# Kernel optimization log

Measured on AMD Instinct MI355X. Metric: run time of the kernel, lower is better.

Reference implementation:

```python
import jax, jax.numpy as jnp
import numpy as np

LN_EPS = 1e-5


def setup_inputs() -> dict:
    key = jax.random.key(0)
    ks = jax.random.split(key, 6)
    B, I, H = 16384, 512, 512
    x = jax.random.normal(ks[0], (B, I), dtype=jnp.float32)
    h_prev = jax.random.normal(ks[1], (B, H), dtype=jnp.float32)
    c_prev = jax.random.normal(ks[2], (B, H), dtype=jnp.float32)
    # packed gate weights in i|f|g|o order (equivalent to 8 separate matmuls)
    W_i = jax.random.normal(ks[3], (I, 4 * H), dtype=jnp.float32) * (1.0 / np.sqrt(I))
    W_h = jax.random.normal(ks[4], (H, 4 * H), dtype=jnp.float32) * (1.0 / np.sqrt(H))
    # biases: b_i=0, b_f=1, b_g=0, b_o=0 as in the torch module
    b = jnp.concatenate([jnp.zeros(H), jnp.ones(H), jnp.zeros(H), jnp.zeros(H)]).astype(jnp.float32)
    ln_weight = jnp.ones((H,), dtype=jnp.float32)
    ln_bias = jnp.zeros((H,), dtype=jnp.float32)
    return {"x": x, "h_prev": h_prev, "c_prev": c_prev, "W_i": W_i, "W_h": W_h,
            "b": b, "ln_weight": ln_weight, "ln_bias": ln_bias}


def layer_norm(h, w, bias):
    mu = jnp.mean(h, axis=-1, keepdims=True)
    var = jnp.var(h, axis=-1, keepdims=True)
    return (h - mu) * jax.lax.rsqrt(var + LN_EPS) * w + bias


def reference(x, h_prev, c_prev, W_i, W_h, b, ln_weight, ln_bias):
    H = h_prev.shape[-1]
    # two fused GEMMs covering all 4 gates: [B, 4H]
    gates = x @ W_i + h_prev @ W_h + b
    i, f, g, o = jnp.split(gates, 4, axis=-1)
    i = jax.nn.sigmoid(i)
    f = jax.nn.sigmoid(f)
    g = jnp.tanh(g)
    o = jax.nn.sigmoid(o)
    c = f * c_prev + i * g
    h = o * jnp.tanh(c)
    h = layer_norm(h, ln_weight, ln_bias)
    return (h, c)
```

## Files before the change

kernel.cpp:

```cpp
#include <hip/hip_runtime.h>
#include <cstdint>
#include <cstddef>

typedef unsigned short ushort_t;
typedef __attribute__((ext_vector_type(8))) short bf16x8;
typedef __attribute__((ext_vector_type(4))) float f32x4;

#define MROWS 16384
#define KDIM  1024
#define NDIM  2048
#define HDIM  512
#define NTILE 16

static __device__ __forceinline__ unsigned short f2bf(float f) {
    unsigned int u = __float_as_uint(f);
    u += 0x7fffu + ((u >> 16) & 1u);
    return (unsigned short)(u >> 16);
}

static __device__ __forceinline__ float sigmoid_f(float x) {
    return 1.0f / (1.0f + __expf(-x));
}
static __device__ __forceinline__ float tanh_f(float x) {
    float t = __expf(2.0f * x);
    return 1.0f - 2.0f / (t + 1.0f);
}

#define PACK_ABLK 2048
#define PACK_STRIDE (PACK_ABLK * 256)
__global__ __launch_bounds__(256) void pack_ab(const float* __restrict__ x,
                                               const float* __restrict__ hp,
                                               const float* __restrict__ Wi,
                                               const float* __restrict__ Wh,
                                               ushort_t* __restrict__ A,
                                               ushort_t* __restrict__ Bt) {
    __shared__ ushort_t sm[64][72];
    const int tid = threadIdx.x;
    if (blockIdx.x < PACK_ABLK) {
        int g = blockIdx.x * 256 + tid;
        float4 v[8];
#pragma unroll
        for (int s = 0; s < 4; ++s) {
            int c = g + s * PACK_STRIDE;
            int row = c >> 7;
            int kc = (c & 127) << 3;
            const float* src = (kc < 512) ? (x + (size_t)row * 512 + kc)
                                          : (hp + (size_t)row * 512 + (kc - 512));
            v[2 * s]     = ((const float4*)src)[0];
            v[2 * s + 1] = ((const float4*)src)[1];
        }
#pragma unroll
        for (int s = 0; s < 4; ++s) {
            int c = g + s * PACK_STRIDE;
            int row = c >> 7;
            int kc = (c & 127) << 3;
            ushort_t o[8] __attribute__((aligned(16)));
            o[0] = f2bf(v[2 * s].x);     o[1] = f2bf(v[2 * s].y);
            o[2] = f2bf(v[2 * s].z);     o[3] = f2bf(v[2 * s].w);
            o[4] = f2bf(v[2 * s + 1].x); o[5] = f2bf(v[2 * s + 1].y);
            o[6] = f2bf(v[2 * s + 1].z); o[7] = f2bf(v[2 * s + 1].w);
            *((uint4*)(A + (size_t)row * KDIM + kc)) = *((const uint4*)o);
        }
    } else {
        int b2 = blockIdx.x - PACK_ABLK;
        int kt = b2 >> 5;
        int ct = b2 & 31;
        const float* W = (kt < 8) ? (Wi + (size_t)(kt * 64) * NDIM)
                                  : (Wh + (size_t)((kt - 8) * 64) * NDIM);
        int c0 = (tid & 15) * 4;
        int r0 = tid >> 4;
#pragma unroll
        for (int r = 0; r < 4; ++r) {
            int krow = r * 16 + r0;
            float4 v = *((const float4*)(W + (size_t)krow * NDIM + ct * 64 + c0));
            sm[krow][c0 + 0] = f2bf(v.x);
            sm[krow][c0 + 1] = f2bf(v.y);
            sm[krow][c0 + 2] = f2bf(v.z);
            sm[krow][c0 + 3] = f2bf(v.w);
        }
        __syncthreads();
        int g = (ct * 64) >> 9;
        int h0 = ct * 64 - g * 512;
#pragma unroll
        for (int q = tid; q < 512; q += 256) {
            int cc = q >> 3;
            int kc = (q & 7) * 8;
            ushort_t o[8] __attribute__((aligned(16)));
#pragma unroll
            for (int j = 0; j < 8; ++j) o[j] = sm[kc + j][cc];
            int np = 4 * (h0 + cc) + g;
            *((uint4*)(Bt + (size_t)np * KDIM + kt * 64 + kc)) = *((const uint4*)o);
        }
    }
}

__global__ __launch_bounds__(512, 2) void gemm_cell(const ushort_t* __restrict__ A,
                                                    const ushort_t* __restrict__ Bt,
                                                    const float* __restrict__ b,
                                                    const float* __restrict__ c_prev,
                                                    float* __restrict__ h_out,
                                                    float* __restrict__ c_out) {
    __shared__ ushort_t lds[2][32768];

    const int tid  = threadIdx.x;
    const int w    = tid >> 6;
    const int lane = tid & 63;
    const int mi   = w >> 2;
    const int nj   = w & 3;
    int bid = blockIdx.x;
    int lid = (bid & 7) * 64 + (bid >> 3);
    const int m0 = (lid >> 3) * 256;
    const int n0 = (lid & 7) * 256;
    const int lr   = lane & 15;
    const int quad = lane >> 4;
    const int sw   = lr & 7;

    const int trow0 = tid >> 3;
    const int chg   = (tid & 7) ^ (trow0 & 7);
    const size_t a_base = (size_t)(m0 + trow0) * KDIM + chg * 8;
    const size_t b_base = (size_t)(n0 + trow0) * KDIM + chg * 8;
    const int    l_base = tid * 16;

#define STAGE_A_SLOT(kt, bufi, r_)                                              \
    __builtin_amdgcn_global_load_lds(                                           \
        (const __attribute__((address_space(1))) void*)(A + a_base +            \
            (size_t)(kt) * 64 + (size_t)(r_) * 64 * KDIM),                      \
        (__attribute__((address_space(3))) void*)((char*)&lds[bufi][0] +        \
            l_base + (r_) * 8192), 16, 0, 0)
#define STAGE_B_SLOT(kt, bufi, r_)                                              \
    __builtin_amdgcn_global_load_lds(                                           \
        (const __attribute__((address_space(1))) void*)(Bt + b_base +           \
            (size_t)(kt) * 64 + (size_t)(r_) * 64 * KDIM),                      \
        (__attribute__((address_space(3))) void*)((char*)&lds[bufi][16384] +    \
            l_base + (r_) * 8192), 16, 0, 0)

    f32x4 acc[8][4];
#pragma unroll
    for (int i = 0; i < 8; ++i)
#pragma unroll
        for (int j = 0; j < 4; ++j) acc[i][j] = (f32x4){0.f, 0.f, 0.f, 0.f};

    STAGE_A_SLOT(0, 0, 0); STAGE_A_SLOT(0, 0, 1); STAGE_A_SLOT(0, 0, 2); STAGE_A_SLOT(0, 0, 3);
    STAGE_B_SLOT(0, 0, 0); STAGE_B_SLOT(0, 0, 1); STAGE_B_SLOT(0, 0, 2); STAGE_B_SLOT(0, 0, 3);
    STAGE_A_SLOT(1, 1, 0); STAGE_A_SLOT(1, 1, 1); STAGE_A_SLOT(1, 1, 2); STAGE_A_SLOT(1, 1, 3);
    STAGE_B_SLOT(1, 1, 0); STAGE_B_SLOT(1, 1, 1); STAGE_B_SLOT(1, 1, 2); STAGE_B_SLOT(1, 1, 3);
    asm volatile("s_waitcnt vmcnt(8)\n\ts_barrier" ::: "memory");

#define TILE(t_, BUF_) do {                                                         \
    const ushort_t* Ab_ = &lds[BUF_][0];                                            \
    const ushort_t* Bb_ = &lds[BUF_][16384];                                        \
    bf16x8 af[4][2], b0v[2][2], b1v[2][2];                                          \
                    \
    _Pragma("unroll")                                                               \
    for (int t2 = 0; t2 < 4; ++t2) {                                                \
        int ra = mi * 128 + t2 * 16 + lr;                                           \
        af[t2][0] = *((const bf16x8*)(Ab_ + (ra * 8 + (quad ^ sw)) * 8));           \
        af[t2][1] = *((const bf16x8*)(Ab_ + (ra * 8 + ((4 + quad) ^ sw)) * 8));     \
    }                                                                               \
    _Pragma("unroll")                                                               \
    for (int j = 0; j < 2; ++j) {                                                   \
        int rb = nj * 64 + j * 16 + lr;                                             \
        b0v[j][0] = *((const bf16x8*)(Bb_ + (rb * 8 + (quad ^ sw)) * 8));           \
        b0v[j][1] = *((const bf16x8*)(Bb_ + (rb * 8 + ((4 + quad) ^ sw)) * 8));     \
    }                                                                               \
    __builtin_amdgcn_s_setprio(1);                                                  \
    _Pragma("unroll")                                                               \
    for (int t2 = 0; t2 < 4; ++t2)                                                  \
        _Pragma("unroll")                                                           \
        for (int j = 0; j < 2; ++j) {                                               \
            acc[t2][j] = __builtin_amdgcn_mfma_f32_16x16x32_bf16(                   \
                af[t2][0], b0v[j][0], acc[t2][j], 0, 0, 0);                         \
            acc[t2][j] = __builtin_amdgcn_mfma_f32_16x16x32_bf16(                   \
                af[t2][1], b0v[j][1], acc[t2][j], 0, 0, 0);                         \
        }                                                                           \
    __builtin_amdgcn_s_setprio(0);                                                  \
    asm volatile("s_barrier" ::: "memory");           \
    if ((t_) < NTILE - 2) { STAGE_A_SLOT((t_) + 2, BUF_, 0);                        \
                            STAGE_A_SLOT((t_) + 2, BUF_, 2); }                      \
                                            \
    _Pragma("unroll")                                                               \
    for (int j = 0; j < 2; ++j) {                                                   \
        int rb = nj * 64 + (j + 2) * 16 + lr;                                       \
        b1v[j][0] = *((const bf16x8*)(Bb_ + (rb * 8 + (quad ^ sw)) * 8));           \
        b1v[j][1] = *((const bf16x8*)(Bb_ + (rb * 8 + ((4 + quad) ^ sw)) * 8));     \
    }                                                                               \
    __builtin_amdgcn_s_setprio(1);                                                  \
    _Pragma("unroll")                                                               \
    for (int t2 = 0; t2 < 4; ++t2)                                                  \
        _Pragma("unroll")                                                           \
        for (int j = 0; j < 2; ++j) {                                               \
            acc[t2][j + 2] = __builtin_amdgcn_mfma_f32_16x16x32_bf16(               \
                af[t2][0], b1v[j][0], acc[t2][j + 2], 0, 0, 0);                     \
            acc[t2][j + 2] = __builtin_amdgcn_mfma_f32_16x16x32_bf16(               \
                af[t2][1], b1v[j][1], acc[t2][j + 2], 0, 0, 0);                     \
        }                                                                           \
    __builtin_amdgcn_s_setprio(0);                                                  \
    asm volatile("s_barrier" ::: "memory");            \
    if ((t_) < NTILE - 2) { STAGE_B_SLOT((t_) + 2, BUF_, 0);                        \
                            STAGE_B_SLOT((t_) + 2, BUF_, 1); }                      \
          \
    _Pragma("unroll")                                                               \
    for (int t2 = 0; t2 < 4; ++t2) {                                                \
        int ra = mi * 128 + (t2 + 4) * 16 + lr;                                     \
        af[t2][0] = *((const bf16x8*)(Ab_ + (ra * 8 + (quad ^ sw)) * 8));           \
        af[t2][1] = *((const bf16x8*)(Ab_ + (ra * 8 + ((4 + quad) ^ sw)) * 8));     \
    }                                                                               \
    __builtin_amdgcn_s_setprio(1);                                                  \
    _Pragma("unroll")                                                               \
    for (int t2 = 0; t2 < 4; ++t2)                                                  \
        _Pragma("unroll")                                                           \
        for (int j = 0; j < 2; ++j) {                                               \
            acc[t2 + 4][j] = __builtin_amdgcn_mfma_f32_16x16x32_bf16(               \
                af[t2][0], b0v[j][0], acc[t2 + 4][j], 0, 0, 0);                     \
            acc[t2 + 4][j] = __builtin_amdgcn_mfma_f32_16x16x32_bf16(               \
                af[t2][1], b0v[j][1], acc[t2 + 4][j], 0, 0, 0);                     \
        }                                                                           \
    __builtin_amdgcn_s_setprio(0);                                                  \
    asm volatile("s_waitcnt lgkmcnt(0)\n\ts_barrier" ::: "memory");         \
    if ((t_) < NTILE - 2) { STAGE_B_SLOT((t_) + 2, BUF_, 2);                        \
                            STAGE_B_SLOT((t_) + 2, BUF_, 3);                        \
                            STAGE_A_SLOT((t_) + 2, BUF_, 1);                        \
                            STAGE_A_SLOT((t_) + 2, BUF_, 3); }                      \
               \
    __builtin_amdgcn_s_setprio(1);                                                  \
    _Pragma("unroll")                                                               \
    for (int t2 = 0; t2 < 4; ++t2)                                                  \
        _Pragma("unroll")                                                           \
        for (int j = 0; j < 2; ++j) {                                               \
            acc[t2 + 4][j + 2] = __builtin_amdgcn_mfma_f32_16x16x32_bf16(           \
                af[t2][0], b1v[j][0], acc[t2 + 4][j + 2], 0, 0, 0);                 \
            acc[t2 + 4][j + 2] = __builtin_amdgcn_mfma_f32_16x16x32_bf16(           \
                af[t2][1], b1v[j][1], acc[t2 + 4][j + 2], 0, 0, 0);                 \
        }                                                                           \
    __builtin_amdgcn_s_setprio(0);                                                  \
    if ((t_) < NTILE - 2) {                                                         \
             \
        asm volatile("s_waitcnt vmcnt(8)\n\ts_barrier" ::: "memory");               \
    } else if ((t_) == NTILE - 2) {                                                 \
        asm volatile("s_waitcnt vmcnt(0)\n\ts_barrier" ::: "memory");               \
    } else {                                                                        \
        asm volatile("s_waitcnt lgkmcnt(0)\n\ts_barrier" ::: "memory");             \
    }                                                                               \
} while (0)

    for (int tp = 0; tp < NTILE / 2; ++tp) {
        TILE(2 * tp, 0);
        TILE(2 * tp + 1, 1);
    }
#undef TILE
#undef STAGE_A_SLOT
#undef STAGE_B_SLOT

    float* scr = (float*)&lds[0][0] + w * 1024;
    const int rr = lane >> 2;
    const int hg0 = ((n0 + nj * 64) >> 2) + (lane & 3) * 4;
    const float4 bi4 = *((const float4*)(b + hg0));
    const float4 bff = *((const float4*)(b + 512 + hg0));
    const float4 bgg = *((const float4*)(b + 1024 + hg0));
    const float4 boo = *((const float4*)(b + 1536 + hg0));
    const float bi[4] = {bi4.x, bi4.y, bi4.z, bi4.w};
    const float bfv[4] = {bff.x, bff.y, bff.z, bff.w};
    const float bg[4] = {bgg.x, bgg.y, bgg.z, bgg.w};
    const float bo[4] = {boo.x, boo.y, boo.z, boo.w};

#pragma unroll
    for (int tm = 0; tm < 8; ++tm) {
#pragma unroll
        for (int tn = 0; tn < 4; ++tn) {
            int c = tn * 16 + lr;
#pragma unroll
            for (int rg = 0; rg < 4; ++rg) {
                int r = quad * 4 + rg;
                int blk = (c >> 2) ^ r;
                scr[r * 64 + blk * 4 + (c & 3)] = acc[tm][tn][rg];
            }
        }
        float4 gv[4];
#pragma unroll
        for (int j = 0; j < 4; ++j) {
            int cb = (lane & 3) * 4 + j;
            gv[j] = *((const float4*)(scr + rr * 64 + (cb ^ rr) * 4));
        }
        int grow = m0 + mi * 128 + tm * 16 + rr;
        float4 cp4 = *((const float4*)(c_prev + (size_t)grow * HDIM + hg0));
        const float cpv[4] = {cp4.x, cp4.y, cp4.z, cp4.w};
        float cn[4], hv[4];
#pragma unroll
        for (int j = 0; j < 4; ++j) {
            float iv = sigmoid_f(gv[j].x + bi[j]);
            float fv = sigmoid_f(gv[j].y + bfv[j]);
            float g2 = tanh_f(gv[j].z + bg[j]);
            float ov = sigmoid_f(gv[j].w + bo[j]);
            cn[j] = fv * cpv[j] + iv * g2;
            hv[j] = ov * tanh_f(cn[j]);
        }
        float4 cno = {cn[0], cn[1], cn[2], cn[3]};
        float4 hvo = {hv[0], hv[1], hv[2], hv[3]};
        *((float4*)(c_out + (size_t)grow * HDIM + hg0)) = cno;
        *((float4*)(h_out + (size_t)grow * HDIM + hg0)) = hvo;
    }
}

__global__ __launch_bounds__(256) void ln_kernel(float* __restrict__ h,
                                                 const float* __restrict__ lw,
                                                 const float* __restrict__ lb) {
    int w = threadIdx.x >> 6;
    int lane = threadIdx.x & 63;
    int r0 = blockIdx.x * 4 + w;
    int r1 = r0 + (MROWS >> 1);
    float* p0 = h + (size_t)r0 * HDIM + lane * 8;
    float* p1 = h + (size_t)r1 * HDIM + lane * 8;
    float4 a0 = ((const float4*)p0)[0];
    float4 c0 = ((const float4*)p0)[1];
    float4 a1 = ((const float4*)p1)[0];
    float4 c1 = ((const float4*)p1)[1];
    const float* wp = lw + lane * 8;
    const float* bp = lb + lane * 8;
    float4 w0 = ((const float4*)wp)[0];
    float4 w1 = ((const float4*)wp)[1];
    float4 b0 = ((const float4*)bp)[0];
    float4 b1 = ((const float4*)bp)[1];

    float s0  = a0.x + a0.y + a0.z + a0.w + c0.x + c0.y + c0.z + c0.w;
    float ss0 = a0.x * a0.x + a0.y * a0.y + a0.z * a0.z + a0.w * a0.w +
                c0.x * c0.x + c0.y * c0.y + c0.z * c0.z + c0.w * c0.w;
    float s1  = a1.x + a1.y + a1.z + a1.w + c1.x + c1.y + c1.z + c1.w;
    float ss1 = a1.x * a1.x + a1.y * a1.y + a1.z * a1.z + a1.w * a1.w +
                c1.x * c1.x + c1.y * c1.y + c1.z * c1.z + c1.w * c1.w;
#pragma unroll
    for (int off = 32; off > 0; off >>= 1) {
        s0  += __shfl_xor(s0, off);
        ss0 += __shfl_xor(ss0, off);
        s1  += __shfl_xor(s1, off);
        ss1 += __shfl_xor(ss1, off);
    }
    float mu0 = s0 * (1.0f / 512.0f);
    float var0 = ss0 * (1.0f / 512.0f) - mu0 * mu0;
    float rstd0 = rsqrtf(var0 + 1e-5f);
    float mu1 = s1 * (1.0f / 512.0f);
    float var1 = ss1 * (1.0f / 512.0f) - mu1 * mu1;
    float rstd1 = rsqrtf(var1 + 1e-5f);

    a0.x = (a0.x - mu0) * rstd0 * w0.x + b0.x;
    a0.y = (a0.y - mu0) * rstd0 * w0.y + b0.y;
    a0.z = (a0.z - mu0) * rstd0 * w0.z + b0.z;
    a0.w = (a0.w - mu0) * rstd0 * w0.w + b0.w;
    c0.x = (c0.x - mu0) * rstd0 * w1.x + b1.x;
    c0.y = (c0.y - mu0) * rstd0 * w1.y + b1.y;
    c0.z = (c0.z - mu0) * rstd0 * w1.z + b1.z;
    c0.w = (c0.w - mu0) * rstd0 * w1.w + b1.w;
    a1.x = (a1.x - mu1) * rstd1 * w0.x + b0.x;
    a1.y = (a1.y - mu1) * rstd1 * w0.y + b0.y;
    a1.z = (a1.z - mu1) * rstd1 * w0.z + b0.z;
    a1.w = (a1.w - mu1) * rstd1 * w0.w + b0.w;
    c1.x = (c1.x - mu1) * rstd1 * w1.x + b1.x;
    c1.y = (c1.y - mu1) * rstd1 * w1.y + b1.y;
    c1.z = (c1.z - mu1) * rstd1 * w1.z + b1.z;
    c1.w = (c1.w - mu1) * rstd1 * w1.w + b1.w;
    ((float4*)p0)[0] = a0;
    ((float4*)p0)[1] = c0;
    ((float4*)p1)[0] = a1;
    ((float4*)p1)[1] = c1;
}

extern "C" void kernel_launch(void* const* d_in, const int* in_sizes, int n_in,
                              void* d_out, int out_size, void* d_ws, size_t ws_size,
                              hipStream_t stream) {
    const float* x      = (const float*)d_in[0];
    const float* h_prev = (const float*)d_in[1];
    const float* c_prev = (const float*)d_in[2];
    const float* W_i    = (const float*)d_in[3];
    const float* W_h    = (const float*)d_in[4];
    const float* b      = (const float*)d_in[5];
    const float* ln_w   = (const float*)d_in[6];
    const float* ln_b   = (const float*)d_in[7];

    float* h_out = (float*)d_out;
    float* c_out = h_out + (size_t)MROWS * HDIM;

    ushort_t* A  = (ushort_t*)d_ws;
    ushort_t* Bt = A + (size_t)MROWS * KDIM;

    pack_ab<<<PACK_ABLK + 512, 256, 0, stream>>>(x, h_prev, W_i, W_h, A, Bt);
    gemm_cell<<<512, 512, 0, stream>>>(A, Bt, b, c_prev, h_out, c_out);
    ln_kernel<<<MROWS / 8, 256, 0, stream>>>(h_out, ln_w, ln_b);
}
```

Baseline: 243.9 us.

## Fuse fp32-to-bf16 activation conversion into GEMM A-tile staging

```diff
diff --git a/kernel.cpp b/kernel.cpp
--- a/kernel.cpp
+++ b/kernel.cpp
@@ -26,75 +26,44 @@
     return 1.0f - 2.0f / (t + 1.0f);
 }
 
-#define PACK_ABLK 2048
-#define PACK_STRIDE (PACK_ABLK * 256)
-__global__ __launch_bounds__(256) void pack_ab(const float* __restrict__ x,
-                                               const float* __restrict__ hp,
-                                               const float* __restrict__ Wi,
+__global__ __launch_bounds__(256) void pack_bt(const float* __restrict__ Wi,
                                                const float* __restrict__ Wh,
-                                               ushort_t* __restrict__ A,
                                                ushort_t* __restrict__ Bt) {
     __shared__ ushort_t sm[64][72];
     const int tid = threadIdx.x;
-    if (blockIdx.x < PACK_ABLK) {
-        int g = blockIdx.x * 256 + tid;
-        float4 v[8];
-#pragma unroll
-        for (int s = 0; s < 4; ++s) {
-            int c = g + s * PACK_STRIDE;
-            int row = c >> 7;
-            int kc = (c & 127) << 3;
-            const float* src = (kc < 512) ? (x + (size_t)row * 512 + kc)
-                                          : (hp + (size_t)row * 512 + (kc - 512));
-            v[2 * s]     = ((const float4*)src)[0];
-            v[2 * s + 1] = ((const float4*)src)[1];
-        }
-#pragma unroll
-        for (int s = 0; s < 4; ++s) {
-            int c = g + s * PACK_STRIDE;
-            int row = c >> 7;
-            int kc = (c & 127) << 3;
-            ushort_t o[8] __attribute__((aligned(16)));
-            o[0] = f2bf(v[2 * s].x);     o[1] = f2bf(v[2 * s].y);
-            o[2] = f2bf(v[2 * s].z);     o[3] = f2bf(v[2 * s].w);
-            o[4] = f2bf(v[2 * s + 1].x); o[5] = f2bf(v[2 * s + 1].y);
-            o[6] = f2bf(v[2 * s + 1].z); o[7] = f2bf(v[2 * s + 1].w);
-            *((uint4*)(A + (size_t)row * KDIM + kc)) = *((const uint4*)o);
-        }
-    } else {
-        int b2 = blockIdx.x - PACK_ABLK;
-        int kt = b2 >> 5;
-        int ct = b2 & 31;
-        const float* W = (kt < 8) ? (Wi + (size_t)(kt * 64) * NDIM)
-                                  : (Wh + (size_t)((kt - 8) * 64) * NDIM);
-        int c0 = (tid & 15) * 4;
-        int r0 = tid >> 4;
-#pragma unroll
-        for (int r = 0; r < 4; ++r) {
-            int krow = r * 16 + r0;
-            float4 v = *((const float4*)(W + (size_t)krow * NDIM + ct * 64 + c0));
-            sm[krow][c0 + 0] = f2bf(v.x);
-            sm[krow][c0 + 1] = f2bf(v.y);
-            sm[krow][c0 + 2] = f2bf(v.z);
-            sm[krow][c0 + 3] = f2bf(v.w);
-        }
-        __syncthreads();
-        int g = (ct * 64) >> 9;
-        int h0 = ct * 64 - g * 512;
-#pragma unroll
-        for (int q = tid; q < 512; q += 256) {
-            int cc = q >> 3;
-            int kc = (q & 7) * 8;
-            ushort_t o[8] __attribute__((aligned(16)));
-#pragma unroll
-            for (int j = 0; j < 8; ++j) o[j] = sm[kc + j][cc];
-            int np = 4 * (h0 + cc) + g;
-            *((uint4*)(Bt + (size_t)np * KDIM + kt * 64 + kc)) = *((const uint4*)o);
-        }
-    }
-}
-
-__global__ __launch_bounds__(512, 2) void gemm_cell(const ushort_t* __restrict__ A,
+    int b2 = blockIdx.x;
+    int kt = b2 >> 5;
+    int ct = b2 & 31;
+    const float* W = (kt < 8) ? (Wi + (size_t)(kt * 64) * NDIM)
+                              : (Wh + (size_t)((kt - 8) * 64) * NDIM);
+    int c0 = (tid & 15) * 4;
+    int r0 = tid >> 4;
+#pragma unroll
+    for (int r = 0; r < 4; ++r) {
+        int krow = r * 16 + r0;
+        float4 v = *((const float4*)(W + (size_t)krow * NDIM + ct * 64 + c0));
+        sm[krow][c0 + 0] = f2bf(v.x);
+        sm[krow][c0 + 1] = f2bf(v.y);
+        sm[krow][c0 + 2] = f2bf(v.z);
+        sm[krow][c0 + 3] = f2bf(v.w);
+    }
+    __syncthreads();
+    int g = (ct * 64) >> 9;
+    int h0 = ct * 64 - g * 512;
+#pragma unroll
+    for (int q = tid; q < 512; q += 256) {
+        int cc = q >> 3;
+        int kc = (q & 7) * 8;
+        ushort_t o[8] __attribute__((aligned(16)));
+#pragma unroll
+        for (int j = 0; j < 8; ++j) o[j] = sm[kc + j][cc];
+        int np = 4 * (h0 + cc) + g;
+        *((uint4*)(Bt + (size_t)np * KDIM + kt * 64 + kc)) = *((const uint4*)o);
+    }
+}
+
+__global__ __launch_bounds__(512, 2) void gemm_cell(const float* __restrict__ xg,
+                                                    const float* __restrict__ hg,
                                                     const ushort_t* __restrict__ Bt,
                                                     const float* __restrict__ b,
                                                     const float* __restrict__ c_prev,
@@ -115,18 +84,15 @@
     const int quad = lane >> 4;
     const int sw   = lr & 7;
 
+    const int arow = tid >> 1;
+    const int half = tid & 1;
+    const int awk  = arow & 7;
+
     const int trow0 = tid >> 3;
     const int chg   = (tid & 7) ^ (trow0 & 7);
-    const size_t a_base = (size_t)(m0 + trow0) * KDIM + chg * 8;
     const size_t b_base = (size_t)(n0 + trow0) * KDIM + chg * 8;
     const int    l_base = tid * 16;
 
-#define STAGE_A_SLOT(kt, bufi, r_)                                              \
-    __builtin_amdgcn_global_load_lds(                                           \
-        (const __attribute__((address_space(1))) void*)(A + a_base +            \
-            (size_t)(kt) * 64 + (size_t)(r_) * 64 * KDIM),                      \
-        (__attribute__((address_space(3))) void*)((char*)&lds[bufi][0] +        \
-            l_base + (r_) * 8192), 16, 0, 0)
 #define STAGE_B_SLOT(kt, bufi, r_)                                              \
     __builtin_amdgcn_global_load_lds(                                           \
         (const __attribute__((address_space(1))) void*)(Bt + b_base +           \
@@ -134,22 +100,62 @@
         (__attribute__((address_space(3))) void*)((char*)&lds[bufi][16384] +    \
             l_base + (r_) * 8192), 16, 0, 0)
 
+#define ALOAD(arv, kt2) do {                                                    \
+    const float* ab_ = ((kt2) < 8)                                              \
+        ? (xg + (size_t)(m0 + arow) * 512 + (kt2) * 64 + half * 32)             \
+        : (hg + (size_t)(m0 + arow) * 512 + ((kt2) - 8) * 64 + half * 32);      \
+    _Pragma("unroll")                                                           \
+    for (int i_ = 0; i_ < 8; ++i_) arv[i_] = ((const float4*)ab_)[i_];          \
+} while (0)
+
+#define CVTW(arv, bufi) do {                                                    \
+    ushort_t* Aw_ = &lds[bufi][0];                                              \
+    _Pragma("unroll")                                                           \
+    for (int j_ = 0; j_ < 4; ++j_) {                                            \
+        uint4 pk_;                                                              \
+        asm("v_cvt_pk_bf16_f32 %0, %1, %2" : "=v"(pk_.x)                        \
+            : "v"(arv[2 * j_].x), "v"(arv[2 * j_].y));                          \
+        asm("v_cvt_pk_bf16_f32 %0, %1, %2" : "=v"(pk_.y)                        \
+            : "v"(arv[2 * j_].z), "v"(arv[2 * j_].w));                          \
+        asm("v_cvt_pk_bf16_f32 %0, %1, %2" : "=v"(pk_.z)                        \
+            : "v"(arv[2 * j_ + 1].x), "v"(arv[2 * j_ + 1].y));                  \
+        asm("v_cvt_pk_bf16_f32 %0, %1, %2" : "=v"(pk_.w)                        \
+            : "v"(arv[2 * j_ + 1].z), "v"(arv[2 * j_ + 1].w));                  \
+        *((uint4*)(Aw_ + (size_t)(arow * 8 + ((half * 4 + j_) ^ awk)) * 8)) = pk_; \
+    }                                                                           \
+} while (0)
+
     f32x4 acc[8][4];
 #pragma unroll
     for (int i = 0; i < 8; ++i)
 #pragma unroll
         for (int j = 0; j < 4; ++j) acc[i][j] = (f32x4){0.f, 0.f, 0.f, 0.f};
 
-    STAGE_A_SLOT(0, 0, 0); STAGE_A_SLOT(0, 0, 1); STAGE_A_SLOT(0, 0, 2); STAGE_A_SLOT(0, 0, 3);
-    STAGE_B_SLOT(0, 0, 0); STAGE_B_SLOT(0, 0, 1); STAGE_B_SLOT(0, 0, 2); STAGE_B_SLOT(0, 0, 3);
-    STAGE_A_SLOT(1, 1, 0); STAGE_A_SLOT(1, 1, 1); STAGE_A_SLOT(1, 1, 2); STAGE_A_SLOT(1, 1, 3);
-    STAGE_B_SLOT(1, 1, 0); STAGE_B_SLOT(1, 1, 1); STAGE_B_SLOT(1, 1, 2); STAGE_B_SLOT(1, 1, 3);
-    asm volatile("s_waitcnt vmcnt(8)\n\ts_barrier" ::: "memory");
+    {
+        float4 ar0v[8], ar1v[8];
+        ALOAD(ar0v, 0);
+        asm volatile("" ::: "memory");
+        STAGE_B_SLOT(0, 0, 0); STAGE_B_SLOT(0, 0, 1);
+        STAGE_B_SLOT(0, 0, 2); STAGE_B_SLOT(0, 0, 3);
+        asm volatile("" ::: "memory");
+        ALOAD(ar1v, 1);
+        asm volatile("" ::: "memory");
+        STAGE_B_SLOT(1, 1, 0); STAGE_B_SLOT(1, 1, 1);
+        STAGE_B_SLOT(1, 1, 2); STAGE_B_SLOT(1, 1, 3);
+        asm volatile("s_waitcnt vmcnt(16)" ::: "memory");
+        CVTW(ar0v, 0);
+        asm volatile("s_waitcnt vmcnt(4)" ::: "memory");
+        CVTW(ar1v, 1);
+        asm volatile("s_waitcnt lgkmcnt(0)\n\ts_barrier" ::: "memory");
+    }
 
 #define TILE(t_, BUF_) do {                                                         \
     const ushort_t* Ab_ = &lds[BUF_][0];                                            \
     const ushort_t* Bb_ = &lds[BUF_][16384];                                        \
     bf16x8 af[4][2], b0v[2][2], b1v[2][2];                                          \
+    float4 arS[8];                                                                  \
+    const bool pf_ = (t_) < NTILE - 2;                                              \
+    if (pf_) ALOAD(arS, (t_) + 2);                    \
                     \
     _Pragma("unroll")                                                               \
     for (int t2 = 0; t2 < 4; ++t2) {                                                \
@@ -174,9 +180,7 @@
                 af[t2][1], b0v[j][1], acc[t2][j], 0, 0, 0);                         \
         }                                                                           \
     __builtin_amdgcn_s_setprio(0);                                                  \
-    asm volatile("s_barrier" ::: "memory");           \
-    if ((t_) < NTILE - 2) { STAGE_A_SLOT((t_) + 2, BUF_, 0);                        \
-                            STAGE_A_SLOT((t_) + 2, BUF_, 2); }                      \
+    asm volatile("s_barrier" ::: "memory");                                 \
                                             \
     _Pragma("unroll")                                                               \
     for (int j = 0; j < 2; ++j) {                                                   \
@@ -196,8 +200,8 @@
         }                                                                           \
     __builtin_amdgcn_s_setprio(0);                                                  \
     asm volatile("s_barrier" ::: "memory");            \
-    if ((t_) < NTILE - 2) { STAGE_B_SLOT((t_) + 2, BUF_, 0);                        \
-                            STAGE_B_SLOT((t_) + 2, BUF_, 1); }                      \
+    if (pf_) { STAGE_B_SLOT((t_) + 2, BUF_, 0); STAGE_B_SLOT((t_) + 2, BUF_, 1);    \
+               STAGE_B_SLOT((t_) + 2, BUF_, 2); STAGE_B_SLOT((t_) + 2, BUF_, 3); }  \
           \
     _Pragma("unroll")                                                               \
     for (int t2 = 0; t2 < 4; ++t2) {                                                \
@@ -216,12 +220,14 @@
                 af[t2][1], b0v[j][1], acc[t2 + 4][j], 0, 0, 0);                     \
         }                                                                           \
     __builtin_amdgcn_s_setprio(0);                                                  \
-    asm volatile("s_waitcnt lgkmcnt(0)\n\ts_barrier" ::: "memory");         \
-    if ((t_) < NTILE - 2) { STAGE_B_SLOT((t_) + 2, BUF_, 2);                        \
-                            STAGE_B_SLOT((t_) + 2, BUF_, 3);                        \
-                            STAGE_A_SLOT((t_) + 2, BUF_, 1);                        \
-                            STAGE_A_SLOT((t_) + 2, BUF_, 3); }                      \
-               \
+                 \
+    if (pf_) {                                                                      \
+        asm volatile("s_waitcnt vmcnt(4) lgkmcnt(0)\n\ts_barrier" ::: "memory");    \
+        CVTW(arS, BUF_);                                \
+    } else {                                                                        \
+        asm volatile("s_waitcnt vmcnt(0) lgkmcnt(0)\n\ts_barrier" ::: "memory");    \
+    }                                                                               \
+                \
     __builtin_amdgcn_s_setprio(1);                                                  \
     _Pragma("unroll")                                                               \
     for (int t2 = 0; t2 < 4; ++t2)                                                  \
@@ -233,13 +239,10 @@
                 af[t2][1], b1v[j][1], acc[t2 + 4][j + 2], 0, 0, 0);                 \
         }                                                                           \
     __builtin_amdgcn_s_setprio(0);                                                  \
-    if ((t_) < NTILE - 2) {                                                         \
-             \
-        asm volatile("s_waitcnt vmcnt(8)\n\ts_barrier" ::: "memory");               \
-    } else if ((t_) == NTILE - 2) {                                                 \
-        asm volatile("s_waitcnt vmcnt(0)\n\ts_barrier" ::: "memory");               \
+    if ((t_) == NTILE - 1) {                                                        \
+        asm volatile("s_waitcnt lgkmcnt(0)\n\ts_barrier" ::: "memory");             \
     } else {                                                                        \
-        asm volatile("s_waitcnt lgkmcnt(0)\n\ts_barrier" ::: "memory");             \
+        asm volatile("s_barrier" ::: "memory");                             \
     }                                                                               \
 } while (0)
 
@@ -248,8 +251,9 @@
         TILE(2 * tp + 1, 1);
     }
 #undef TILE
-#undef STAGE_A_SLOT
 #undef STAGE_B_SLOT
+#undef ALOAD
+#undef CVTW
 
     float* scr = (float*)&lds[0][0] + w * 1024;
     const int rr = lane >> 2;
@@ -378,10 +382,9 @@
     float* h_out = (float*)d_out;
     float* c_out = h_out + (size_t)MROWS * HDIM;
 
-    ushort_t* A  = (ushort_t*)d_ws;
-    ushort_t* Bt = A + (size_t)MROWS * KDIM;
-
-    pack_ab<<<PACK_ABLK + 512, 256, 0, stream>>>(x, h_prev, W_i, W_h, A, Bt);
-    gemm_cell<<<512, 512, 0, stream>>>(A, Bt, b, c_prev, h_out, c_out);
+    ushort_t* Bt = (ushort_t*)d_ws;
+
+    pack_bt<<<512, 256, 0, stream>>>(W_i, W_h, Bt);
+    gemm_cell<<<512, 512, 0, stream>>>(x, h_prev, Bt, b, c_prev, h_out, c_out);
     ln_kernel<<<MROWS / 8, 256, 0, stream>>>(h_out, ln_w, ln_b);
 }
```

After: 317.0 us. +30.0%, slower.
